# Performance work log

Measured on AMD Instinct MI355X. Metric: run time of the kernel, lower is better.

The kernel has to match this reference:

```python
import jax, jax.numpy as jnp
import numpy as np

N = 100000   # nodes
E = 800000   # edges
FEAT = 384   # raw feature dim (match layer input)
IN = 64      # in_dim
H = 64       # hidden_dim


def setup_inputs() -> dict:
    key = jax.random.key(0)
    ks = jax.random.split(key, 9)
    x = jax.random.normal(ks[0], (N, FEAT), dtype=jnp.float32)
    edge_index = jax.random.randint(ks[1], (2, E), 0, N)
    edge_weight = jax.random.uniform(ks[2], (E,), dtype=jnp.float32)
    Wm = jax.random.normal(ks[3], (FEAT, IN), dtype=jnp.float32) * (FEAT ** -0.5)
    bm = jnp.zeros((IN,), dtype=jnp.float32)
    W1 = jax.random.normal(ks[4], (IN, H), dtype=jnp.float32) * (IN ** -0.5)
    b1 = jnp.zeros((H,), dtype=jnp.float32)
    W2 = jax.random.normal(ks[5], (H, H), dtype=jnp.float32) * (H ** -0.5)
    b2 = jnp.zeros((H,), dtype=jnp.float32)
    return {"x": x, "edge_index": edge_index, "edge_weight": edge_weight,
            "Wm": Wm, "bm": bm, "W1": W1, "b1": b1, "W2": W2, "b2": b2}


def _gcn_conv(x, W, b, src, dst, ew, num_nodes):
    """PyG GCNConv: out = D^{-1/2} (A+I) D^{-1/2} (x W) + b."""
    # add self loops with weight 1
    loop = jnp.arange(num_nodes, dtype=src.dtype)
    row = jnp.concatenate([src, loop])          # source (message sender)
    col = jnp.concatenate([dst, loop])          # destination (aggregation target)
    w = jnp.concatenate([ew, jnp.ones((num_nodes,), dtype=x.dtype)])
    # symmetric normalization: deg computed over destination
    deg = jax.ops.segment_sum(w, col, num_segments=num_nodes)
    dinv = jnp.where(deg > 0, jax.lax.rsqrt(deg), 0.0)
    norm = dinv[row] * w * dinv[col]            # [E+N]
    h = x @ W                                   # [N, out]
    msg = h[row] * norm[:, None]                # gather + scale
    out = jax.ops.segment_sum(msg, col, num_segments=num_nodes)  # scatter-add
    return out + b


def reference(x, edge_index, edge_weight, Wm, bm, W1, b1, W2, b2):
    src, dst = edge_index[0], edge_index[1]
    if x.shape[-1] != IN:
        x = x @ Wm + bm                         # match: Linear(384, in_dim)
    h = _gcn_conv(x, W1, b1, src, dst, edge_weight, N)
    h = jax.nn.relu(h)                          # relu between layers only
    out = _gcn_conv(h, W2, b2, src, dst, edge_weight, N)
    return out
```

## Files before the change

kernel.cpp:

```cpp
#include <hip/hip_runtime.h>


#define NN 100000
#define NE 800000
#define BC 32

typedef unsigned short u16;
typedef __attribute__((ext_vector_type(8))) short short8;
typedef __attribute__((ext_vector_type(4))) float f4;
typedef __attribute__((ext_vector_type(8))) unsigned short u16x8;

__device__ __forceinline__ u16 f2b(float f) {
    unsigned int x = __float_as_uint(f);
    x += 0x7fffu + ((x >> 16) & 1u);
    return (u16)(x >> 16);
}
__device__ __forceinline__ float b2f(u16 u) {
    return __uint_as_float(((unsigned int)u) << 16);
}

__global__ __launch_bounds__(256) void degwf_k(const int* __restrict__ ei,
                                               const float* __restrict__ ew,
                                               float* __restrict__ deg,
                                               const float* __restrict__ Wm,
                                               const float* __restrict__ W1,
                                               float* __restrict__ Wf) {
    __shared__ u16 Blds[2 * 256 * 8];
    int tid = threadIdx.x, bid = blockIdx.x;
    if (bid < 3125) {
        int e = bid * 256 + tid;
        atomicAdd(&deg[ei[NE + e]], ew[e]);
        return;
    }
    for (int idx = tid; idx < 2 * 256; idx += 256) {
        int kt = idx >> 8, rem = idx & 255;
        int ct = rem >> 6, ln = rem & 63;
        int kb = kt * 32 + (ln >> 4) * 8;
        int col = ct * 16 + (ln & 15);
#pragma unroll
        for (int j = 0; j < 8; j++)
            Blds[idx * 8 + j] = f2b(W1[(kb + j) * 64 + col]);
    }
    __syncthreads();
    int wave = tid >> 6, lane = tid & 63;
    int rowtile = (bid - 3125) * 4 + wave;
    int rowbase = rowtile * 16;
    int m = lane & 15, quad = lane >> 4;
    f4 acc[4];
#pragma unroll
    for (int ct = 0; ct < 4; ct++) acc[ct] = 0.0f;
    const short8* Bfrag = (const short8*)Blds;
#pragma unroll
    for (int kt = 0; kt < 2; kt++) {
        const f4* p = (const f4*)&Wm[(size_t)(rowbase + m) * 64 + kt * 32 + quad * 8];
        f4 v0 = p[0], v1 = p[1];
        short8 af;
#pragma unroll
        for (int j = 0; j < 4; j++) {
            af[j]     = (short)f2b(v0[j]);
            af[4 + j] = (short)f2b(v1[j]);
        }
#pragma unroll
        for (int ct = 0; ct < 4; ct++)
            acc[ct] = __builtin_amdgcn_mfma_f32_16x16x32_bf16(af, Bfrag[(kt * 4 + ct) * 64 + lane], acc[ct], 0, 0, 0);
    }
#pragma unroll
    for (int ct = 0; ct < 4; ct++) {
        int col = ct * 16 + m;
#pragma unroll
        for (int r = 0; r < 4; r++)
            Wf[(size_t)(rowbase + quad * 4 + r) * 64 + col] = acc[ct][r];
    }
}

__global__ __launch_bounds__(256) void fillgemm_k(const int* __restrict__ ei,
                                                  const float* __restrict__ ew,
                                                  const float* __restrict__ deg,
                                                  int* __restrict__ count,
                                                  int2* __restrict__ e2,
                                                  const float* __restrict__ x,
                                                  const float* __restrict__ Wf,
                                                  u16* __restrict__ hb) {
    __shared__ u16 Blds[4 * 256 * 8];
    int tid = threadIdx.x, bid = blockIdx.x;
    if (bid >= 1563) {
        int e = (bid - 1563) * 256 + tid;
        int src = ei[e];
        int dst = ei[NE + e];
        float coef = rsqrtf(deg[src] + 1.0f) * ew[e] * rsqrtf(deg[dst] + 1.0f);
        int pos = atomicAdd(&count[dst], 1);
        if (pos < BC)
            e2[(size_t)dst * BC + pos] = make_int2(src, __float_as_int(coef));
        return;
    }
    int wave = tid >> 6, lane = tid & 63;
    int rowtile = bid * 4 + wave;
    bool act = rowtile < 6250;
    int rowbase = (act ? rowtile : 6249) * 16;
    int m = lane & 15, quad = lane >> 4;

    f4 acc[4];
#pragma unroll
    for (int ct = 0; ct < 4; ct++) acc[ct] = 0.0f;
    const short8* Bfrag = (const short8*)Blds;

#pragma unroll
    for (int chunk = 0; chunk < 3; chunk++) {
        for (int idx = tid; idx < 4 * 256; idx += 256) {
            int ktl = idx >> 8, rem = idx & 255;
            int ct = rem >> 6, ln = rem & 63;
            int kb = (chunk * 4 + ktl) * 32 + (ln >> 4) * 8;
            int col = ct * 16 + (ln & 15);
#pragma unroll
            for (int j = 0; j < 8; j++)
                Blds[idx * 8 + j] = f2b(Wf[(size_t)(kb + j) * 64 + col]);
        }
        __syncthreads();
#pragma unroll
        for (int ktl = 0; ktl < 4; ktl++) {
            const f4* p = (const f4*)&x[(size_t)(rowbase + m) * 384 + (chunk * 4 + ktl) * 32 + quad * 8];
            f4 v0 = p[0], v1 = p[1];
            short8 af;
#pragma unroll
            for (int j = 0; j < 4; j++) {
                af[j]     = (short)f2b(v0[j]);
                af[4 + j] = (short)f2b(v1[j]);
            }
#pragma unroll
            for (int ct = 0; ct < 4; ct++)
                acc[ct] = __builtin_amdgcn_mfma_f32_16x16x32_bf16(af, Bfrag[(ktl * 4 + ct) * 64 + lane], acc[ct], 0, 0, 0);
        }
        __syncthreads();
    }

    if (act) {
#pragma unroll
        for (int ct = 0; ct < 4; ct++) {
            int col = ct * 16 + m;
#pragma unroll
            for (int r = 0; r < 4; r++)
                hb[(size_t)(rowbase + quad * 4 + r) * 64 + col] = f2b(acc[ct][r]);
        }
    }
}

__device__ __forceinline__ void gatherC(const int2* __restrict__ eb, int cntv, int dst,
                                        const u16* __restrict__ hb, int ch,
                                        float* __restrict__ acc, float& cs) {
    const int4* eb4 = (const int4*)eb;
    for (int i = 0; i < cntv; i += 8) {
        int4 q[4];
#pragma unroll
        for (int p = 0; p < 4; p++) q[p] = eb4[(i >> 1) + p];
        int s[8];
        float c[8];
#pragma unroll
        for (int p = 0; p < 4; p++) {
            int t0 = i + 2 * p;
            bool v0 = t0 < cntv, v1 = (t0 + 1) < cntv;
            s[2 * p]     = v0 ? q[p].x : dst;
            c[2 * p]     = v0 ? __int_as_float(q[p].y) : 0.0f;
            s[2 * p + 1] = v1 ? q[p].z : dst;
            c[2 * p + 1] = v1 ? __int_as_float(q[p].w) : 0.0f;
        }
        u16x8 hv[8];
#pragma unroll
        for (int t = 0; t < 8; t++)
            hv[t] = *(const u16x8*)&hb[(size_t)s[t] * 64 + ch * 8];
#pragma unroll
        for (int t = 0; t < 8; t++) {
            cs += c[t];
#pragma unroll
            for (int j = 0; j < 8; j++)
                acc[j] = fmaf(c[t], b2f(hv[t][j]), acc[j]);
        }
    }
}

__global__ __launch_bounds__(256) void gather1_k(const int2* __restrict__ e2,
                                                 const int* __restrict__ count,
                                                 const float* __restrict__ deg,
                                                 const u16* __restrict__ hb,
                                                 const float* __restrict__ bm,
                                                 const float* __restrict__ W1,
                                                 const float* __restrict__ b1,
                                                 u16* __restrict__ aggb) {
    __shared__ float bmw1s[64];
    int tid = threadIdx.x;
    if (tid < 64) {
        float a = 0.0f;
#pragma unroll 8
        for (int k = 0; k < 64; k++) a = fmaf(bm[k], W1[k * 64 + tid], a);
        bmw1s[tid] = a;
    }
    __syncthreads();

    int rt = tid >> 3, ch = tid & 7;
    int dst = blockIdx.x * 32 + rt;
    int cntv = min(count[dst], BC);
    float dd = 1.0f / (deg[dst] + 1.0f);
    u16x8 hs = *(const u16x8*)&hb[(size_t)dst * 64 + ch * 8];

    float acc[8] = {0, 0, 0, 0, 0, 0, 0, 0};
    float cs = 0.0f;
    gatherC(&e2[(size_t)dst * BC], cntv, dst, hb, ch, acc, cs);

    float s = dd + cs;
    u16x8 o;
#pragma unroll
    for (int j = 0; j < 8; j++) {
        float v = fmaf(dd, b2f(hs[j]), acc[j]);
        o[j] = f2b(fmaxf(fmaf(s, bmw1s[ch * 8 + j], v) + b1[ch * 8 + j], 0.0f));
    }
    ((u16x8*)aggb)[(size_t)dst * 8 + ch] = o;
}

__global__ __launch_bounds__(256) void g2gemm_k(const int2* __restrict__ e2,
                                                const int* __restrict__ count,
                                                const float* __restrict__ deg,
                                                const u16* __restrict__ aggb,
                                                const float* __restrict__ W2,
                                                const float* __restrict__ b2,
                                                float* __restrict__ out) {
    __shared__ u16 Wlds[4096];
    __shared__ u16 Atile[32][72];
    int tid = threadIdx.x;
    for (int idx = tid; idx < 2 * 256; idx += 256) {
        int kt = idx >> 8, rem = idx & 255;
        int ct = rem >> 6, ln = rem & 63;
        int kb = kt * 32 + (ln >> 4) * 8;
        int col = ct * 16 + (ln & 15);
#pragma unroll
        for (int j = 0; j < 8; j++)
            Wlds[idx * 8 + j] = f2b(W2[(size_t)(kb + j) * 64 + col]);
    }

    int rt = tid >> 3, ch = tid & 7;
    int dst = blockIdx.x * 32 + rt;
    int cntv = min(count[dst], BC);
    float dd = 1.0f / (deg[dst] + 1.0f);
    u16x8 hs = *(const u16x8*)&aggb[(size_t)dst * 64 + ch * 8];

    float acc[8] = {0, 0, 0, 0, 0, 0, 0, 0};
    float cs = 0.0f;
    gatherC(&e2[(size_t)dst * BC], cntv, dst, aggb, ch, acc, cs);

    u16x8 o;
#pragma unroll
    for (int j = 0; j < 8; j++)
        o[j] = f2b(fmaf(dd, b2f(hs[j]), acc[j]));
    *(u16x8*)&Atile[rt][ch * 8] = o;
    __syncthreads();

    if (tid >= 128) return;
    int wave = tid >> 6, lane = tid & 63;
    int m = lane & 15, quad = lane >> 4;
    int rowoff = wave * 16;
    f4 cacc[4];
#pragma unroll
    for (int ct = 0; ct < 4; ct++) cacc[ct] = 0.0f;
    const short8* Bfrag = (const short8*)Wlds;
#pragma unroll
    for (int kt = 0; kt < 2; kt++) {
        short8 af = *(const short8*)&Atile[rowoff + m][kt * 32 + quad * 8];
#pragma unroll
        for (int ct = 0; ct < 4; ct++)
            cacc[ct] = __builtin_amdgcn_mfma_f32_16x16x32_bf16(af, Bfrag[(kt * 4 + ct) * 64 + lane], cacc[ct], 0, 0, 0);
    }
    int rowbase = blockIdx.x * 32 + rowoff;
#pragma unroll
    for (int ct = 0; ct < 4; ct++) {
        int col = ct * 16 + m;
        float bc = b2[col];
#pragma unroll
        for (int rr = 0; rr < 4; rr++)
            out[(size_t)(rowbase + quad * 4 + rr) * 64 + col] = cacc[ct][rr] + bc;
    }
}

extern "C" void kernel_launch(void* const* d_in, const int* in_sizes, int n_in,
                              void* d_out, int out_size, void* d_ws, size_t ws_size,
                              hipStream_t stream) {
    const float* x  = (const float*)d_in[0];
    const int*   ei = (const int*)d_in[1];
    const float* ew = (const float*)d_in[2];
    const float* Wm = (const float*)d_in[3];
    const float* bm = (const float*)d_in[4];
    const float* W1 = (const float*)d_in[5];
    const float* b1 = (const float*)d_in[6];
    const float* W2 = (const float*)d_in[7];
    const float* b2 = (const float*)d_in[8];
    float* out = (float*)d_out;

    char*  w     = (char*)d_ws;
    float* deg   = (float*)(w);
    int*   count = (int*)(w + 400000);
    float* Wf    = (float*)(w + (1 << 20));
    int2*  e2    = (int2*)(w + (4 << 20));
    u16*   hb    = (u16*)(w + (64u << 20));
    u16*   aggb  = (u16*)(w + (80u << 20));

    hipMemsetAsync(w, 0, 800000, stream);
    degwf_k<<<3131, 256, 0, stream>>>(ei, ew, deg, Wm, W1, Wf);
    fillgemm_k<<<4688, 256, 0, stream>>>(ei, ew, deg, count, e2, x, Wf, hb);
    gather1_k<<<3125, 256, 0, stream>>>(e2, count, deg, hb, bm, W1, b1, aggb);
    g2gemm_k<<<3125, 256, 0, stream>>>(e2, count, deg, aggb, W2, b2, out);
}
```

Before: 379.2 us.

## Restructure GCN pipeline: defer W1 multiply after aggregation, store raw edge weights

Stops folding Wm·W1 into one fused weight. The x@Wm projection now runs in the same kernel as the degree and edge-bucket fill, storing raw edge weights instead of normalized coefficients. A new scale kernel applies the source-side rsqrt(deg) to the fp32 projection, and the first-layer gather kernel now performs the W1 GEMM with MFMA after aggregation, applying the destination scaling, bias and ReLU in its epilogue. This removes the dependency that forced the edge fill to wait for the degree pass, at the cost of an extra fp32 intermediate round trip (writing t32 and reading it back) and an additional launch.

```diff
diff --git a/kernel.cpp b/kernel.cpp
--- a/kernel.cpp
+++ b/kernel.cpp
@@ -19,82 +19,30 @@
     return __uint_as_float(((unsigned int)u) << 16);
 }
 
-__global__ __launch_bounds__(256) void degwf_k(const int* __restrict__ ei,
-                                               const float* __restrict__ ew,
-                                               float* __restrict__ deg,
-                                               const float* __restrict__ Wm,
-                                               const float* __restrict__ W1,
-                                               float* __restrict__ Wf) {
-    __shared__ u16 Blds[2 * 256 * 8];
+__global__ __launch_bounds__(256) void mega_k(const int* __restrict__ ei,
+                                              const float* __restrict__ ew,
+                                              float* __restrict__ deg,
+                                              int* __restrict__ count,
+                                              int2* __restrict__ e2,
+                                              const float* __restrict__ x,
+                                              const float* __restrict__ Wm,
+                                              const float* __restrict__ bm,
+                                              float* __restrict__ t32) {
+    __shared__ u16 Blds[4 * 256 * 8];
     int tid = threadIdx.x, bid = blockIdx.x;
     if (bid < 3125) {
         int e = bid * 256 + tid;
-        atomicAdd(&deg[ei[NE + e]], ew[e]);
+        int src = ei[e];
+        int dst = ei[NE + e];
+        float wv = ew[e];
+        atomicAdd(&deg[dst], wv);
+        int pos = atomicAdd(&count[dst], 1);
+        if (pos < BC)
+            e2[(size_t)dst * BC + pos] = make_int2(src, __float_as_int(wv));
         return;
     }
-    for (int idx = tid; idx < 2 * 256; idx += 256) {
-        int kt = idx >> 8, rem = idx & 255;
-        int ct = rem >> 6, ln = rem & 63;
-        int kb = kt * 32 + (ln >> 4) * 8;
-        int col = ct * 16 + (ln & 15);
-#pragma unroll
-        for (int j = 0; j < 8; j++)
-            Blds[idx * 8 + j] = f2b(W1[(kb + j) * 64 + col]);
-    }
-    __syncthreads();
     int wave = tid >> 6, lane = tid & 63;
     int rowtile = (bid - 3125) * 4 + wave;
-    int rowbase = rowtile * 16;
-    int m = lane & 15, quad = lane >> 4;
-    f4 acc[4];
-#pragma unroll
-    for (int ct = 0; ct < 4; ct++) acc[ct] = 0.0f;
-    const short8* Bfrag = (const short8*)Blds;
-#pragma unroll
-    for (int kt = 0; kt < 2; kt++) {
-        const f4* p = (const f4*)&Wm[(size_t)(rowbase + m) * 64 + kt * 32 + quad * 8];
-        f4 v0 = p[0], v1 = p[1];
-        short8 af;
-#pragma unroll
-        for (int j = 0; j < 4; j++) {
-            af[j]     = (short)f2b(v0[j]);
-            af[4 + j] = (short)f2b(v1[j]);
-        }
-#pragma unroll
-        for (int ct = 0; ct < 4; ct++)
-            acc[ct] = __builtin_amdgcn_mfma_f32_16x16x32_bf16(af, Bfrag[(kt * 4 + ct) * 64 + lane], acc[ct], 0, 0, 0);
-    }
-#pragma unroll
-    for (int ct = 0; ct < 4; ct++) {
-        int col = ct * 16 + m;
-#pragma unroll
-        for (int r = 0; r < 4; r++)
-            Wf[(size_t)(rowbase + quad * 4 + r) * 64 + col] = acc[ct][r];
-    }
-}
-
-__global__ __launch_bounds__(256) void fillgemm_k(const int* __restrict__ ei,
-                                                  const float* __restrict__ ew,
-                                                  const float* __restrict__ deg,
-                                                  int* __restrict__ count,
-                                                  int2* __restrict__ e2,
-                                                  const float* __restrict__ x,
-                                                  const float* __restrict__ Wf,
-                                                  u16* __restrict__ hb) {
-    __shared__ u16 Blds[4 * 256 * 8];
-    int tid = threadIdx.x, bid = blockIdx.x;
-    if (bid >= 1563) {
-        int e = (bid - 1563) * 256 + tid;
-        int src = ei[e];
-        int dst = ei[NE + e];
-        float coef = rsqrtf(deg[src] + 1.0f) * ew[e] * rsqrtf(deg[dst] + 1.0f);
-        int pos = atomicAdd(&count[dst], 1);
-        if (pos < BC)
-            e2[(size_t)dst * BC + pos] = make_int2(src, __float_as_int(coef));
-        return;
-    }
-    int wave = tid >> 6, lane = tid & 63;
-    int rowtile = bid * 4 + wave;
     bool act = rowtile < 6250;
     int rowbase = (act ? rowtile : 6249) * 16;
     int m = lane & 15, quad = lane >> 4;
@@ -113,7 +61,7 @@
             int col = ct * 16 + (ln & 15);
 #pragma unroll
             for (int j = 0; j < 8; j++)
-                Blds[idx * 8 + j] = f2b(Wf[(size_t)(kb + j) * 64 + col]);
+                Blds[idx * 8 + j] = f2b(Wm[(size_t)(kb + j) * 64 + col]);
         }
         __syncthreads();
 #pragma unroll
@@ -137,16 +85,35 @@
 #pragma unroll
         for (int ct = 0; ct < 4; ct++) {
             int col = ct * 16 + m;
+            float bmv = bm[col];
 #pragma unroll
             for (int r = 0; r < 4; r++)
-                hb[(size_t)(rowbase + quad * 4 + r) * 64 + col] = f2b(acc[ct][r]);
-        }
-    }
-}
-
-__device__ __forceinline__ void gatherC(const int2* __restrict__ eb, int cntv, int dst,
+                t32[(size_t)(rowbase + quad * 4 + r) * 64 + col] = acc[ct][r] + bmv;
+        }
+    }
+}
+
+__global__ __launch_bounds__(256) void scale_k(const float* __restrict__ deg,
+                                               const float* __restrict__ t32,
+                                               u16* __restrict__ ts) {
+    int tid = threadIdx.x;
+    int rt = tid >> 3, ch = tid & 7;
+    int row = blockIdx.x * 32 + rt;
+    float rsd = rsqrtf(deg[row] + 1.0f);
+    const f4* p = (const f4*)&t32[(size_t)row * 64 + ch * 8];
+    f4 v0 = p[0], v1 = p[1];
+    u16x8 o;
+#pragma unroll
+    for (int j = 0; j < 4; j++) {
+        o[j]     = f2b(rsd * v0[j]);
+        o[4 + j] = f2b(rsd * v1[j]);
+    }
+    ((u16x8*)ts)[(size_t)row * 8 + ch] = o;
+}
+
+__device__ __forceinline__ void gatherR(const int2* __restrict__ eb, int cntv, int dst,
                                         const u16* __restrict__ hb, int ch,
-                                        float* __restrict__ acc, float& cs) {
+                                        float* __restrict__ acc) {
     const int4* eb4 = (const int4*)eb;
     for (int i = 0; i < cntv; i += 8) {
         int4 q[4];
@@ -169,7 +136,6 @@
             hv[t] = *(const u16x8*)&hb[(size_t)s[t] * 64 + ch * 8];
 #pragma unroll
         for (int t = 0; t < 8; t++) {
-            cs += c[t];
 #pragma unroll
             for (int j = 0; j < 8; j++)
                 acc[j] = fmaf(c[t], b2f(hv[t][j]), acc[j]);
@@ -177,42 +143,75 @@
     }
 }
 
-__global__ __launch_bounds__(256) void gather1_k(const int2* __restrict__ e2,
-                                                 const int* __restrict__ count,
-                                                 const float* __restrict__ deg,
-                                                 const u16* __restrict__ hb,
-                                                 const float* __restrict__ bm,
-                                                 const float* __restrict__ W1,
-                                                 const float* __restrict__ b1,
-                                                 u16* __restrict__ aggb) {
-    __shared__ float bmw1s[64];
+__device__ __forceinline__ void fillW(u16* Wlds, const float* __restrict__ W, int tid) {
+    for (int idx = tid; idx < 2 * 256; idx += 256) {
+        int kt = idx >> 8, rem = idx & 255;
+        int ct = rem >> 6, ln = rem & 63;
+        int kb = kt * 32 + (ln >> 4) * 8;
+        int col = ct * 16 + (ln & 15);
+#pragma unroll
+        for (int j = 0; j < 8; j++)
+            Wlds[idx * 8 + j] = f2b(W[(size_t)(kb + j) * 64 + col]);
+    }
+}
+
+__global__ __launch_bounds__(256) void g1gemm_k(const int2* __restrict__ e2,
+                                                const int* __restrict__ count,
+                                                const float* __restrict__ deg,
+                                                const u16* __restrict__ ts,
+                                                const float* __restrict__ W1,
+                                                const float* __restrict__ b1,
+                                                u16* __restrict__ aggb) {
+    __shared__ u16 Wlds[4096];
+    __shared__ u16 Atile[32][72];
+    __shared__ float rsds[32];
     int tid = threadIdx.x;
-    if (tid < 64) {
-        float a = 0.0f;
-#pragma unroll 8
-        for (int k = 0; k < 64; k++) a = fmaf(bm[k], W1[k * 64 + tid], a);
-        bmw1s[tid] = a;
-    }
-    __syncthreads();
+    fillW(Wlds, W1, tid);
 
     int rt = tid >> 3, ch = tid & 7;
     int dst = blockIdx.x * 32 + rt;
     int cntv = min(count[dst], BC);
-    float dd = 1.0f / (deg[dst] + 1.0f);
-    u16x8 hs = *(const u16x8*)&hb[(size_t)dst * 64 + ch * 8];
+    float rsdd = rsqrtf(deg[dst] + 1.0f);
+    u16x8 hs = *(const u16x8*)&ts[(size_t)dst * 64 + ch * 8];
 
     float acc[8] = {0, 0, 0, 0, 0, 0, 0, 0};
-    float cs = 0.0f;
-    gatherC(&e2[(size_t)dst * BC], cntv, dst, hb, ch, acc, cs);
-
-    float s = dd + cs;
+    gatherR(&e2[(size_t)dst * BC], cntv, dst, ts, ch, acc);
+
     u16x8 o;
 #pragma unroll
-    for (int j = 0; j < 8; j++) {
-        float v = fmaf(dd, b2f(hs[j]), acc[j]);
-        o[j] = f2b(fmaxf(fmaf(s, bmw1s[ch * 8 + j], v) + b1[ch * 8 + j], 0.0f));
-    }
-    ((u16x8*)aggb)[(size_t)dst * 8 + ch] = o;
+    for (int j = 0; j < 8; j++)
+        o[j] = f2b(rsdd * (acc[j] + b2f(hs[j])));
+    *(u16x8*)&Atile[rt][ch * 8] = o;
+    if (ch == 0) rsds[rt] = rsdd;
+    __syncthreads();
+
+    if (tid >= 128) return;
+    int wave = tid >> 6, lane = tid & 63;
+    int m = lane & 15, quad = lane >> 4;
+    int rowoff = wave * 16;
+    f4 cacc[4];
+#pragma unroll
+    for (int ct = 0; ct < 4; ct++) cacc[ct] = 0.0f;
+    const short8* Bfrag = (const short8*)Wlds;
+#pragma unroll
+    for (int kt = 0; kt < 2; kt++) {
+        short8 af = *(const short8*)&Atile[rowoff + m][kt * 32 + quad * 8];
+#pragma unroll
+        for (int ct = 0; ct < 4; ct++)
+            cacc[ct] = __builtin_amdgcn_mfma_f32_16x16x32_bf16(af, Bfrag[(kt * 4 + ct) * 64 + lane], cacc[ct], 0, 0, 0);
+    }
+    int rowbase = blockIdx.x * 32 + rowoff;
+#pragma unroll
+    for (int ct = 0; ct < 4; ct++) {
+        int col = ct * 16 + m;
+        float bb = b1[col];
+#pragma unroll
+        for (int rr = 0; rr < 4; rr++) {
+            int rl = rowoff + quad * 4 + rr;
+            float v = fmaxf(cacc[ct][rr] + bb, 0.0f);
+            aggb[(size_t)(rowbase + quad * 4 + rr) * 64 + col] = f2b(rsds[rl] * v);
+        }
+    }
 }
 
 __global__ __launch_bounds__(256) void g2gemm_k(const int2* __restrict__ e2,
@@ -225,30 +224,21 @@
     __shared__ u16 Wlds[4096];
     __shared__ u16 Atile[32][72];
     int tid = threadIdx.x;
-    for (int idx = tid; idx < 2 * 256; idx += 256) {
-        int kt = idx >> 8, rem = idx & 255;
-        int ct = rem >> 6, ln = rem & 63;
-        int kb = kt * 32 + (ln >> 4) * 8;
-        int col = ct * 16 + (ln & 15);
-#pragma unroll
-        for (int j = 0; j < 8; j++)
-            Wlds[idx * 8 + j] = f2b(W2[(size_t)(kb + j) * 64 + col]);
-    }
+    fillW(Wlds, W2, tid);
 
     int rt = tid >> 3, ch = tid & 7;
     int dst = blockIdx.x * 32 + rt;
     int cntv = min(count[dst], BC);
-    float dd = 1.0f / (deg[dst] + 1.0f);
+    float rsdd = rsqrtf(deg[dst] + 1.0f);
     u16x8 hs = *(const u16x8*)&aggb[(size_t)dst * 64 + ch * 8];
 
     float acc[8] = {0, 0, 0, 0, 0, 0, 0, 0};
-    float cs = 0.0f;
-    gatherC(&e2[(size_t)dst * BC], cntv, dst, aggb, ch, acc, cs);
+    gatherR(&e2[(size_t)dst * BC], cntv, dst, aggb, ch, acc);
 
     u16x8 o;
 #pragma unroll
     for (int j = 0; j < 8; j++)
-        o[j] = f2b(fmaf(dd, b2f(hs[j]), acc[j]));
+        o[j] = f2b(rsdd * (acc[j] + b2f(hs[j])));
     *(u16x8*)&Atile[rt][ch * 8] = o;
     __syncthreads();
 
@@ -295,14 +285,14 @@
     char*  w     = (char*)d_ws;
     float* deg   = (float*)(w);
     int*   count = (int*)(w + 400000);
-    float* Wf    = (float*)(w + (1 << 20));
-    int2*  e2    = (int2*)(w + (4 << 20));
-    u16*   hb    = (u16*)(w + (64u << 20));
+    int2*  e2    = (int2*)(w + (4u << 20));
+    float* t32   = (float*)(w + (32u << 20));
+    u16*   ts    = (u16*)(w + (64u << 20));
     u16*   aggb  = (u16*)(w + (80u << 20));
 
     hipMemsetAsync(w, 0, 800000, stream);
-    degwf_k<<<3131, 256, 0, stream>>>(ei, ew, deg, Wm, W1, Wf);
-    fillgemm_k<<<4688, 256, 0, stream>>>(ei, ew, deg, count, e2, x, Wf, hb);
-    gather1_k<<<3125, 256, 0, stream>>>(e2, count, deg, hb, bm, W1, b1, aggb);
+    mega_k<<<4688, 256, 0, stream>>>(ei, ew, deg, count, e2, x, Wm, bm, t32);
+    scale_k<<<3125, 256, 0, stream>>>(deg, t32, ts);
+    g1gemm_k<<<3125, 256, 0, stream>>>(e2, count, deg, ts, W1, b1, aggb);
     g2gemm_k<<<3125, 256, 0, stream>>>(e2, count, deg, aggb, W2, b2, out);
 }
```

Result: slower. 389.1 us (+2.6%).
